# Kernel optimization log

Hardware: AMD Instinct MI355X
Metric: run time of the kernel (lower is better)

The kernel has to match this reference:

```python
import jax, jax.numpy as jnp
import numpy as np

B, IN, OUT = 384, 512, 384  # B must equal OUT (broadcast in original sigma_3 + diag(sigma_bias))


def setup_inputs() -> dict:
    key = jax.random.key(0)
    k1, k2, k3, k4 = jax.random.split(key, 4)
    mu = jax.random.normal(k1, (B, IN), dtype=jnp.float32)
    sigma = jax.random.uniform(k2, (B, IN, IN), dtype=jnp.float32)
    # nn.Linear weight: normal(0, 0.1); bias filled with 1e-4
    W = 0.1 * jax.random.normal(k3, (OUT, IN), dtype=jnp.float32)
    b = jnp.full((OUT,), 1e-4, dtype=jnp.float32)
    # sigma_weight ~ U(-12, -2.2); sigma_bias = ones * bias(True)
    sigma_weight = jax.random.uniform(k4, (OUT, IN), minval=-12.0, maxval=-2.2, dtype=jnp.float32)
    sigma_bias = jnp.ones((OUT,), dtype=jnp.float32)
    return {"mu": mu, "sigma": sigma, "W": W, "b": b,
            "sigma_weight": sigma_weight, "sigma_bias": sigma_bias}


def reference(mu, sigma, W, b, sigma_weight, sigma_bias):
    sp = jnp.log1p(jnp.exp(sigma_weight))            # softplus(sigma_weight), [OUT, IN]
    mu_f = mu @ W.T + b                              # [B, OUT]
    # sigma_1: diag( sum_i sigma[b,i,i] * sp[o,i] )  (equivalent to the torch
    # diag_embed / batched-matmul / diagonal chain, without the [B,OUT,IN,IN] blowup)
    diag_sigma = jnp.diagonal(sigma, axis1=1, axis2=2)   # [B, IN]
    s1 = jnp.einsum('bi,oi->bo', diag_sigma, sp)         # [B, OUT]
    # sigma_2 = W @ sigma @ W^T, dense part
    s2 = jnp.einsum('oi,bij,pj->bop', W, sigma, W)       # [B, OUT, OUT]
    # sigma_3 = sp @ mu^2 + diag(sigma_bias)  ([B,OUT] + [OUT,OUT], valid since B==OUT)
    s3 = jnp.square(mu) @ sp.T + jnp.diag(sigma_bias)    # [B, OUT]
    eye = jnp.eye(sp.shape[0], dtype=mu.dtype)
    sigma_out = (s1 + s3)[:, :, None] * eye + s2         # [B, OUT, OUT]
    return mu_f, sigma_out
```

## Files before the change

kernel.cpp:

```cpp
#include <hip/hip_runtime.h>
#include <hip/hip_bf16.h>
#include <math.h>

#define Bn   384
#define INn  512
#define OUTn 384

typedef __bf16 bf16x8 __attribute__((ext_vector_type(8)));
typedef __bf16 bf16x4 __attribute__((ext_vector_type(4)));
typedef float  f32x4  __attribute__((ext_vector_type(4)));

__device__ __bf16 g_Wbf[OUTn * INn];
__device__ float  g_sp [OUTn * INn];
__device__ float  g_d  [Bn * OUTn];

__global__ __launch_bounds__(256) void prep_kernel(const float* __restrict__ W,
                                                   const float* __restrict__ sw) {
    int idx = blockIdx.x * 256 + threadIdx.x;
    if (idx < OUTn * INn) {
        g_Wbf[idx] = (__bf16)W[idx];
        float x = sw[idx];
        g_sp[idx] = (x > 20.f) ? x : log1pf(expf(x));
    }
}

__global__ __launch_bounds__(256) void k2_kernel(const float* __restrict__ mu,
                                                 const float* __restrict__ sigma,
                                                 const float* __restrict__ W,
                                                 const float* __restrict__ bias,
                                                 const float* __restrict__ sbias,
                                                 float* __restrict__ out_muf) {
    const int b  = blockIdx.x;
    const int oq = blockIdx.y;
    __shared__ __align__(16) float muL[INn];
    __shared__ __align__(16) float tL[INn];
    const int tid = threadIdx.x;
    for (int i = tid; i < INn; i += 256) {
        float m = mu[b * INn + i];
        muL[i] = m;
        tL[i] = sigma[(size_t)b * (INn * INn) + (size_t)i * (INn + 1)] + m * m;
    }
    __syncthreads();
    const int wave = tid >> 6, lane = tid & 63;
    const float4* Mr = (const float4*)muL;
    const float4* Tr = (const float4*)tL;
    float4 m0 = Mr[lane * 2], m1 = Mr[lane * 2 + 1];
    float4 t0 = Tr[lane * 2], t1 = Tr[lane * 2 + 1];
#pragma unroll 4
    for (int ow = 0; ow < 24; ++ow) {
        const int o = oq * 96 + wave * 24 + ow;
        const float4* Wr = (const float4*)(W + (size_t)o * INn);
        const float4* Sr = (const float4*)(g_sp + (size_t)o * INn);
        float4 w0 = Wr[lane * 2], w1 = Wr[lane * 2 + 1];
        float4 s0 = Sr[lane * 2], s1 = Sr[lane * 2 + 1];
        float mf = w0.x * m0.x + w0.y * m0.y + w0.z * m0.z + w0.w * m0.w
                 + w1.x * m1.x + w1.y * m1.y + w1.z * m1.z + w1.w * m1.w;
        float dd = s0.x * t0.x + s0.y * t0.y + s0.z * t0.z + s0.w * t0.w
                 + s1.x * t1.x + s1.y * t1.y + s1.z * t1.z + s1.w * t1.w;
#pragma unroll
        for (int off = 32; off; off >>= 1) {
            mf += __shfl_xor(mf, off, 64);
            dd += __shfl_xor(dd, off, 64);
        }
        if (lane == 0) {
            out_muf[b * OUTn + o] = mf + bias[o];
            g_d[b * OUTn + o] = dd + (o == b ? sbias[o] : 0.f);
        }
    }
}

__global__ __launch_bounds__(512, 4) void wsw_kernel(const float* __restrict__ sigma,
                                                     float* __restrict__ outS) {
    __shared__ __bf16 Ut[64][INn + 8];

    const int ptile = blockIdx.x;
    const int b     = blockIdx.y;
    const int tid   = threadIdx.x;
    const int wave  = tid >> 6;
    const int lane  = tid & 63;
    const int quad  = lane >> 4;
    const int l15   = lane & 15;
    const int p0    = ptile * 64;

    const float* sigb = sigma + (size_t)b * (INn * INn);

    {
        const int i_base = wave * 64;
        f32x4 acc[4][4];
#pragma unroll
        for (int mi = 0; mi < 4; ++mi)
#pragma unroll
            for (int nf = 0; nf < 4; ++nf) acc[mi][nf] = (f32x4){0.f, 0.f, 0.f, 0.f};

        for (int kc = 0; kc < INn; kc += 32) {
            bf16x8 afr[4];
#pragma unroll
            for (int mi = 0; mi < 4; ++mi) {
                const float* ap = sigb + (size_t)(i_base + mi * 16 + l15) * INn + kc + quad * 8;
                float4 a0 = *(const float4*)ap;
                float4 a1 = *(const float4*)(ap + 4);
                bf16x8 t;
                t[0] = (__bf16)a0.x; t[1] = (__bf16)a0.y; t[2] = (__bf16)a0.z; t[3] = (__bf16)a0.w;
                t[4] = (__bf16)a1.x; t[5] = (__bf16)a1.y; t[6] = (__bf16)a1.z; t[7] = (__bf16)a1.w;
                afr[mi] = t;
            }
#pragma unroll
            for (int nf = 0; nf < 4; ++nf) {
                const __bf16* bp = g_Wbf + (size_t)(p0 + nf * 16 + l15) * INn + kc + quad * 8;
                bf16x8 bfr = *(const bf16x8*)bp;
#pragma unroll
                for (int mi = 0; mi < 4; ++mi)
                    acc[mi][nf] = __builtin_amdgcn_mfma_f32_16x16x32_bf16(afr[mi], bfr, acc[mi][nf], 0, 0, 0);
            }
        }
#pragma unroll
        for (int mi = 0; mi < 4; ++mi) {
            int ib = i_base + mi * 16 + quad * 4;
#pragma unroll
            for (int nf = 0; nf < 4; ++nf) {
                int p = nf * 16 + l15;
                bf16x4 v;
                v[0] = (__bf16)acc[mi][nf][0];
                v[1] = (__bf16)acc[mi][nf][1];
                v[2] = (__bf16)acc[mi][nf][2];
                v[3] = (__bf16)acc[mi][nf][3];
                *(bf16x4*)&Ut[p][ib] = v;
            }
        }
    }
    __syncthreads();

    {
        const int o_base = wave * 48;
        f32x4 acc[3][4];
#pragma unroll
        for (int mi = 0; mi < 3; ++mi)
#pragma unroll
            for (int nf = 0; nf < 4; ++nf) acc[mi][nf] = (f32x4){0.f, 0.f, 0.f, 0.f};

        for (int kc = 0; kc < INn; kc += 32) {
            bf16x8 afr[3];
#pragma unroll
            for (int mi = 0; mi < 3; ++mi) {
                const __bf16* ap = g_Wbf + (size_t)(o_base + mi * 16 + l15) * INn + kc + quad * 8;
                afr[mi] = *(const bf16x8*)ap;
            }
#pragma unroll
            for (int nf = 0; nf < 4; ++nf) {
                bf16x8 bfr = *(const bf16x8*)&Ut[nf * 16 + l15][kc + quad * 8];
#pragma unroll
                for (int mi = 0; mi < 3; ++mi)
                    acc[mi][nf] = __builtin_amdgcn_mfma_f32_16x16x32_bf16(afr[mi], bfr, acc[mi][nf], 0, 0, 0);
            }
        }
        float* outb = outS + (size_t)b * (OUTn * OUTn);
#pragma unroll
        for (int mi = 0; mi < 3; ++mi) {
            int o_r = o_base + mi * 16 + quad * 4;
#pragma unroll
            for (int nf = 0; nf < 4; ++nf) {
                int p = p0 + nf * 16 + l15;
#pragma unroll
                for (int r = 0; r < 4; ++r) {
                    int o = o_r + r;
                    float v = acc[mi][nf][r];
                    if (o == p) v += g_d[b * OUTn + o];
                    outb[(size_t)o * OUTn + p] = v;
                }
            }
        }
    }
}

extern "C" void kernel_launch(void* const* d_in, const int* in_sizes, int n_in,
                              void* d_out, int out_size, void* d_ws, size_t ws_size,
                              hipStream_t stream) {
    const float* mu    = (const float*)d_in[0];
    const float* sigma = (const float*)d_in[1];
    const float* W     = (const float*)d_in[2];
    const float* bias  = (const float*)d_in[3];
    const float* sw    = (const float*)d_in[4];
    const float* sbias = (const float*)d_in[5];

    float* out     = (float*)d_out;
    float* out_muf = out;
    float* out_sig = out + Bn * OUTn;

    prep_kernel<<<(OUTn * INn + 255) / 256, 256, 0, stream>>>(W, sw);
    k2_kernel<<<dim3(Bn, 4), 256, 0, stream>>>(mu, sigma, W, bias, sbias, out_muf);
    wsw_kernel<<<dim3(6, Bn), 512, 0, stream>>>(sigma, out_sig);
}
```

Measured before the change: 1.047 ms.

## Split sigma·W^T into separate pass storing bf16 intermediate to avoid recompute

The fused kernel recomputed the sigma·W^T product and re-read all of sigma for each of six output column tiles. A new passA computes the bf16 intermediate U once per batch element and stores it in a global buffer, also capturing sigma's diagonal for the k2 kernel. passB loads its U slice and performs only the second GEMM. This trades a ~150 MB intermediate write and read plus an extra launch for removing redundant sigma traffic and duplicated MFMA work.

Result: faster. 930.5 us (-11.1%).

```diff
diff --git a/kernel.cpp b/kernel.cpp
--- a/kernel.cpp
+++ b/kernel.cpp
@@ -13,6 +13,8 @@
 __device__ __bf16 g_Wbf[OUTn * INn];
 __device__ float  g_sp [OUTn * INn];
 __device__ float  g_d  [Bn * OUTn];
+__device__ float  g_t  [Bn * INn];
+__device__ __bf16 g_U  [(size_t)Bn * OUTn * INn];
 
 __global__ __launch_bounds__(256) void prep_kernel(const float* __restrict__ W,
                                                    const float* __restrict__ sw) {
@@ -24,8 +26,78 @@
     }
 }
 
+__global__ __launch_bounds__(512, 4) void passA_kernel(const float* __restrict__ sigma) {
+    __shared__ __bf16 As[64][INn + 8];
+
+    const int it   = blockIdx.x;
+    const int b    = blockIdx.y;
+    const int tid  = threadIdx.x;
+    const int wave = tid >> 6, lane = tid & 63;
+    const int quad = lane >> 4, l15 = lane & 15;
+    const int i0   = it * 64;
+
+    const float* sigb = sigma + (size_t)b * (INn * INn) + (size_t)i0 * INn;
+
+#pragma unroll
+    for (int k = 0; k < 8; ++k) {
+        const int r = k * 8 + wave;
+        const float* rp = sigb + (size_t)r * INn + lane * 8;
+        float4 a0 = *(const float4*)rp;
+        float4 a1 = *(const float4*)(rp + 4);
+        bf16x8 t;
+        t[0]=(__bf16)a0.x; t[1]=(__bf16)a0.y; t[2]=(__bf16)a0.z; t[3]=(__bf16)a0.w;
+        t[4]=(__bf16)a1.x; t[5]=(__bf16)a1.y; t[6]=(__bf16)a1.z; t[7]=(__bf16)a1.w;
+        *(bf16x8*)&As[r][lane * 8] = t;
+        const int ig = i0 + r;
+        if ((ig >> 3) == lane) {
+            const int c = ig & 7;
+            float dv = (c==0)?a0.x:(c==1)?a0.y:(c==2)?a0.z:(c==3)?a0.w
+                     :(c==4)?a1.x:(c==5)?a1.y:(c==6)?a1.z:a1.w;
+            g_t[b * INn + ig] = dv;
+        }
+    }
+    __syncthreads();
+
+    const int p_base = wave * 48;
+    f32x4 acc[4][3];
+#pragma unroll
+    for (int mi = 0; mi < 4; ++mi)
+#pragma unroll
+        for (int nf = 0; nf < 3; ++nf) acc[mi][nf] = (f32x4){0.f, 0.f, 0.f, 0.f};
+
+    for (int kc = 0; kc < INn; kc += 32) {
+        bf16x8 afr[4];
+#pragma unroll
+        for (int mi = 0; mi < 4; ++mi)
+            afr[mi] = *(const bf16x8*)&As[mi * 16 + l15][kc + quad * 8];
+#pragma unroll
+        for (int nf = 0; nf < 3; ++nf) {
+            const __bf16* bp = g_Wbf + (size_t)(p_base + nf * 16 + l15) * INn + kc + quad * 8;
+            bf16x8 bfr = *(const bf16x8*)bp;
+#pragma unroll
+            for (int mi = 0; mi < 4; ++mi)
+                acc[mi][nf] = __builtin_amdgcn_mfma_f32_16x16x32_bf16(afr[mi], bfr, acc[mi][nf], 0, 0, 0);
+        }
+    }
+
+    __bf16* Ub = g_U + (size_t)b * (OUTn * INn);
+#pragma unroll
+    for (int mi = 0; mi < 4; ++mi) {
+        const int ib = i0 + mi * 16 + quad * 4;
+#pragma unroll
+        for (int nf = 0; nf < 3; ++nf) {
+            const int p = p_base + nf * 16 + l15;
+            bf16x4 v;
+            v[0] = (__bf16)acc[mi][nf][0];
+            v[1] = (__bf16)acc[mi][nf][1];
+            v[2] = (__bf16)acc[mi][nf][2];
+            v[3] = (__bf16)acc[mi][nf][3];
+            *(bf16x4*)(Ub + (size_t)p * INn + ib) = v;
+        }
+    }
+}
+
 __global__ __launch_bounds__(256) void k2_kernel(const float* __restrict__ mu,
-                                                 const float* __restrict__ sigma,
                                                  const float* __restrict__ W,
                                                  const float* __restrict__ bias,
                                                  const float* __restrict__ sbias,
@@ -38,7 +110,7 @@
     for (int i = tid; i < INn; i += 256) {
         float m = mu[b * INn + i];
         muL[i] = m;
-        tL[i] = sigma[(size_t)b * (INn * INn) + (size_t)i * (INn + 1)] + m * m;
+        tL[i] = g_t[b * INn + i] + m * m;
     }
     __syncthreads();
     const int wave = tid >> 6, lane = tid & 63;
@@ -69,104 +141,60 @@
     }
 }
 
-__global__ __launch_bounds__(512, 4) void wsw_kernel(const float* __restrict__ sigma,
-                                                     float* __restrict__ outS) {
+__global__ __launch_bounds__(512, 4) void passB_kernel(float* __restrict__ outS) {
     __shared__ __bf16 Ut[64][INn + 8];
 
     const int ptile = blockIdx.x;
     const int b     = blockIdx.y;
     const int tid   = threadIdx.x;
-    const int wave  = tid >> 6;
-    const int lane  = tid & 63;
-    const int quad  = lane >> 4;
-    const int l15   = lane & 15;
+    const int wave  = tid >> 6, lane = tid & 63;
+    const int quad  = lane >> 4, l15 = lane & 15;
     const int p0    = ptile * 64;
 
-    const float* sigb = sigma + (size_t)b * (INn * INn);
-
-    {
-        const int i_base = wave * 64;
-        f32x4 acc[4][4];
-#pragma unroll
-        for (int mi = 0; mi < 4; ++mi)
-#pragma unroll
-            for (int nf = 0; nf < 4; ++nf) acc[mi][nf] = (f32x4){0.f, 0.f, 0.f, 0.f};
-
-        for (int kc = 0; kc < INn; kc += 32) {
-            bf16x8 afr[4];
-#pragma unroll
-            for (int mi = 0; mi < 4; ++mi) {
-                const float* ap = sigb + (size_t)(i_base + mi * 16 + l15) * INn + kc + quad * 8;
-                float4 a0 = *(const float4*)ap;
-                float4 a1 = *(const float4*)(ap + 4);
-                bf16x8 t;
-                t[0] = (__bf16)a0.x; t[1] = (__bf16)a0.y; t[2] = (__bf16)a0.z; t[3] = (__bf16)a0.w;
-                t[4] = (__bf16)a1.x; t[5] = (__bf16)a1.y; t[6] = (__bf16)a1.z; t[7] = (__bf16)a1.w;
-                afr[mi] = t;
-            }
-#pragma unroll
-            for (int nf = 0; nf < 4; ++nf) {
-                const __bf16* bp = g_Wbf + (size_t)(p0 + nf * 16 + l15) * INn + kc + quad * 8;
-                bf16x8 bfr = *(const bf16x8*)bp;
-#pragma unroll
-                for (int mi = 0; mi < 4; ++mi)
-                    acc[mi][nf] = __builtin_amdgcn_mfma_f32_16x16x32_bf16(afr[mi], bfr, acc[mi][nf], 0, 0, 0);
-            }
-        }
-#pragma unroll
-        for (int mi = 0; mi < 4; ++mi) {
-            int ib = i_base + mi * 16 + quad * 4;
-#pragma unroll
-            for (int nf = 0; nf < 4; ++nf) {
-                int p = nf * 16 + l15;
-                bf16x4 v;
-                v[0] = (__bf16)acc[mi][nf][0];
-                v[1] = (__bf16)acc[mi][nf][1];
-                v[2] = (__bf16)acc[mi][nf][2];
-                v[3] = (__bf16)acc[mi][nf][3];
-                *(bf16x4*)&Ut[p][ib] = v;
-            }
-        }
+    const __bf16* Ub = g_U + ((size_t)b * OUTn + p0) * INn;
+#pragma unroll
+    for (int k = 0; k < 8; ++k) {
+        const int r = k * 8 + wave;
+        *(bf16x8*)&Ut[r][lane * 8] = *(const bf16x8*)(Ub + (size_t)r * INn + lane * 8);
     }
     __syncthreads();
 
-    {
-        const int o_base = wave * 48;
-        f32x4 acc[3][4];
-#pragma unroll
-        for (int mi = 0; mi < 3; ++mi)
-#pragma unroll
-            for (int nf = 0; nf < 4; ++nf) acc[mi][nf] = (f32x4){0.f, 0.f, 0.f, 0.f};
-
-        for (int kc = 0; kc < INn; kc += 32) {
-            bf16x8 afr[3];
-#pragma unroll
-            for (int mi = 0; mi < 3; ++mi) {
-                const __bf16* ap = g_Wbf + (size_t)(o_base + mi * 16 + l15) * INn + kc + quad * 8;
-                afr[mi] = *(const bf16x8*)ap;
-            }
-#pragma unroll
-            for (int nf = 0; nf < 4; ++nf) {
-                bf16x8 bfr = *(const bf16x8*)&Ut[nf * 16 + l15][kc + quad * 8];
-#pragma unroll
-                for (int mi = 0; mi < 3; ++mi)
-                    acc[mi][nf] = __builtin_amdgcn_mfma_f32_16x16x32_bf16(afr[mi], bfr, acc[mi][nf], 0, 0, 0);
-            }
-        }
-        float* outb = outS + (size_t)b * (OUTn * OUTn);
+    const int o_base = wave * 48;
+    f32x4 acc[3][4];
+#pragma unroll
+    for (int mi = 0; mi < 3; ++mi)
+#pragma unroll
+        for (int nf = 0; nf < 4; ++nf) acc[mi][nf] = (f32x4){0.f, 0.f, 0.f, 0.f};
+
+    for (int kc = 0; kc < INn; kc += 32) {
+        bf16x8 afr[3];
 #pragma unroll
         for (int mi = 0; mi < 3; ++mi) {
-            int o_r = o_base + mi * 16 + quad * 4;
-#pragma unroll
-            for (int nf = 0; nf < 4; ++nf) {
-                int p = p0 + nf * 16 + l15;
-#pragma unroll
-                for (int r = 0; r < 4; ++r) {
-                    int o = o_r + r;
-                    float v = acc[mi][nf][r];
-                    if (o == p) v += g_d[b * OUTn + o];
-                    outb[(size_t)o * OUTn + p] = v;
-                }
+            const __bf16* ap = g_Wbf + (size_t)(o_base + mi * 16 + l15) * INn + kc + quad * 8;
+            afr[mi] = *(const bf16x8*)ap;
+        }
+#pragma unroll
+        for (int nf = 0; nf < 4; ++nf) {
+            bf16x8 bfr = *(const bf16x8*)&Ut[nf * 16 + l15][kc + quad * 8];
+#pragma unroll
+            for (int mi = 0; mi < 3; ++mi)
+                acc[mi][nf] = __builtin_amdgcn_mfma_f32_16x16x32_bf16(afr[mi], bfr, acc[mi][nf], 0, 0, 0);
+        }
+    }
+
+    float* outb = outS + (size_t)b * (OUTn * OUTn);
+#pragma unroll
+    for (int mi = 0; mi < 3; ++mi) {
+        const int o_r = o_base + mi * 16 + quad * 4;
+#pragma unroll
+        for (int nf = 0; nf < 4; ++nf) {
+            const int p = p0 + nf * 16 + l15;
+#pragma unroll
+            for (int r = 0; r < 4; ++r) {
+                const int o = o_r + r;
+                float v = acc[mi][nf][r];
+                if (o == p) v += g_d[b * OUTn + o];
+                outb[(size_t)o * OUTn + p] = v;
             }
         }
     }
@@ -187,6 +215,7 @@
     float* out_sig = out + Bn * OUTn;
 
     prep_kernel<<<(OUTn * INn + 255) / 256, 256, 0, stream>>>(W, sw);
-    k2_kernel<<<dim3(Bn, 4), 256, 0, stream>>>(mu, sigma, W, bias, sbias, out_muf);
-    wsw_kernel<<<dim3(6, Bn), 512, 0, stream>>>(sigma, out_sig);
-}
+    passA_kernel<<<dim3(8, Bn), 512, 0, stream>>>(sigma);
+    k2_kernel<<<dim3(Bn, 4), 256, 0, stream>>>(mu, W, bias, sbias, out_muf);
+    passB_kernel<<<dim3(6, Bn), 512, 0, stream>>>(out_sig);
+}
```
